# Kernel tuning notes

Measured on AMD Instinct MI355X. Metric: run time of the kernel, lower is better.

The kernel has to match this reference:

```python
import math
import jax, jax.numpy as jnp
import numpy as np

DIM = 1024
QK_DIM = 200
HIDDEN = 2 * DIM  # expansion_factor = 2
N = 8192


def setup_inputs() -> dict:
    key = jax.random.key(0)
    ks = jax.random.split(key, 8)
    s = 0.02
    return {
        "x": jax.random.normal(ks[0], (N, DIM), dtype=jnp.float32),
        "W_hidden": jax.random.normal(ks[1], (DIM, 2 * HIDDEN), dtype=jnp.float32) * s,
        "b_hidden": jnp.zeros((2 * HIDDEN,), dtype=jnp.float32),
        "W_qk": jax.random.normal(ks[2], (DIM, QK_DIM), dtype=jnp.float32) * s,
        "b_qk": jnp.zeros((QK_DIM,), dtype=jnp.float32),
        "gamma": 1.0 + jax.random.normal(ks[3], (2, QK_DIM), dtype=jnp.float32) * s,
        "beta": jnp.zeros((2, QK_DIM), dtype=jnp.float32),
        "W_out": jax.random.normal(ks[4], (HIDDEN, DIM), dtype=jnp.float32) * s,
        "b_out": jnp.zeros((DIM,), dtype=jnp.float32),
    }


def reference(x, W_hidden, b_hidden, W_qk, b_qk, gamma, beta, W_out, b_out):
    # to_hidden: Linear(dim -> 2*hidden) + SiLU, then chunk into v, gate
    hid = jax.nn.silu(x @ W_hidden + b_hidden)        # [N, 2H]
    v, gate = jnp.split(hid, 2, axis=-1)              # [N, H] each
    # to_qk: Linear(dim -> qk_dim) + SiLU
    qk = jax.nn.silu(x @ W_qk + b_qk)                 # [N, qk]
    # OffsetScale (heads=2): per-head affine on the shared qk
    q = qk * gamma[0] + beta[0]                       # [N, qk]
    k = qk * gamma[1] + beta[1]                       # [N, qk]
    # scores scaled by sqrt(dim) (module uses self.dim, not qk_dim)
    sim = (q @ k.T) * (1.0 / math.sqrt(x.shape[-1]))  # [N, N]
    # ReLU-squared attention (no softmax); dropout=0.0 -> identity
    attn = jnp.square(jax.nn.relu(sim))
    out = attn @ v                                    # [N, H]
    out = out * gate
    out = out @ W_out + b_out                         # [N, dim]
    # add_residual=True in this module multiplies by x
    return out * x
```

## Files before the change

kernel.cpp:

```cpp
#include <hip/hip_runtime.h>
#include <stdint.h>


typedef __bf16 bf16x8 __attribute__((ext_vector_type(8)));
typedef float f32x4 __attribute__((ext_vector_type(4)));

__device__ __forceinline__ uint16_t f2bf(float f) {
  uint32_t u = __builtin_bit_cast(uint32_t, f);
  u += 0x7fffu + ((u >> 16) & 1u);
  return (uint16_t)(u >> 16);
}
__device__ __forceinline__ float silu_f(float s) {
  return s / (1.f + __expf(-s));
}

__device__ __forceinline__ void gload16(const void* g, void* l) {
  __builtin_amdgcn_global_load_lds(
      (__attribute__((address_space(1))) void*)const_cast<void*>(g),
      (__attribute__((address_space(3))) void*)l, 16, 0, 0);
}


__global__ void cast_to_bf16(const float* __restrict__ in, uint16_t* __restrict__ out, int n4) {
  int i = blockIdx.x * blockDim.x + threadIdx.x;
  if (i < n4) {
    float4 f = ((const float4*)in)[i];
    ushort4 o;
    o.x = f2bf(f.x); o.y = f2bf(f.y); o.z = f2bf(f.z); o.w = f2bf(f.w);
    ((ushort4*)out)[i] = o;
  }
}

__global__ void transpose_cast_pad(const float* __restrict__ in, uint16_t* __restrict__ out,
                                   int R, int C, int Cp) {
  __shared__ float tile[32][33];
  int cb = blockIdx.x * 32;
  int rb = blockIdx.y * 32;
  int tx = threadIdx.x;
  int ty = threadIdx.y;
#pragma unroll
  for (int i = 0; i < 4; ++i) {
    int r = rb + ty + i * 8;
    int c = cb + tx;
    tile[ty + i * 8][tx] = (c < C) ? in[(size_t)r * C + c] : 0.f;
  }
  __syncthreads();
#pragma unroll
  for (int i = 0; i < 4; ++i) {
    int c = cb + ty + i * 8;
    if (c < Cp) out[(size_t)c * R + rb + tx] = f2bf(tile[tx][ty + i * 8]);
  }
}

__global__ void k_sum(uint16_t* __restrict__ P0, const uint16_t* __restrict__ P1,
                      const uint16_t* __restrict__ g, int n8) {
  int i = blockIdx.x * blockDim.x + threadIdx.x;
  if (i < n8) {
    bf16x8 a = ((const bf16x8*)P0)[i];
    bf16x8 b = ((const bf16x8*)P1)[i];
    bf16x8 gg = ((const bf16x8*)g)[i];
    bf16x8 o;
#pragma unroll
    for (int e = 0; e < 8; ++e)
      o[e] = (__bf16)(((float)a[e] + (float)b[e]) * (float)gg[e]);
    ((bf16x8*)P0)[i] = o;
  }
}


struct EpiParams {
  const float* bias;
  const float* bias2;
  const float* g0;
  const float* b0;
  const float* g1;
  const float* b1;
  const uint16_t* gate;
  const float* x;
  uint16_t* o16a;
  uint16_t* o16b;
  uint16_t* oq;
  uint16_t* ok;
  float* o32;
};

#define ET(T_, WS_, RS_, CA_, CB_, NA_, NB_)                                   \
  do {                                                                         \
    const int kp_ = (((T_) + 3) & (NT - 1)) * 32;                              \
    uint16_t* sd_ = SH + (WS_) * 16384 + wave * 512;                           \
    gload16(gA0 + kp_, sd_);                                                   \
    gload16(gA1 + kp_, sd_ + 4096);                                            \
    gload16(gB0 + kp_, sd_ + 8192);                                            \
    gload16(gB1 + kp_, sd_ + 12288);                                           \
    const uint16_t* rb_ = SH + (RS_) * 16384;                                  \
    _Pragma("unroll") for (int j_ = 0; j_ < 4; ++j_)                           \
        NB_[j_] = *(const bf16x8*)(rb_ + rdB + j_ * 512);                      \
    _Pragma("unroll") for (int i_ = 0; i_ < 8; ++i_)                           \
        NA_[i_] = *(const bf16x8*)(rb_ + rdA + i_ * 512);                      \
    __builtin_amdgcn_sched_barrier(0);                                         \
    __builtin_amdgcn_s_setprio(1);                                             \
    _Pragma("unroll") for (int i_ = 0; i_ < 8; ++i_)                           \
      _Pragma("unroll") for (int j_ = 0; j_ < 4; ++j_)                         \
          acc[i_][j_] = __builtin_amdgcn_mfma_f32_16x16x32_bf16(               \
              CA_[i_], CB_[j_], acc[i_][j_], 0, 0, 0);                         \
    __builtin_amdgcn_s_setprio(0);                                             \
    asm volatile("s_waitcnt vmcnt(4)" ::: "memory");                           \
    __builtin_amdgcn_sched_barrier(0);                                         \
    __builtin_amdgcn_s_barrier();                                              \
    __builtin_amdgcn_sched_barrier(0);                                         \
  } while (0)

#define ENGINE256()                                                            \
  do {                                                                         \
    _Pragma("unroll") for (int s_ = 0; s_ < 3; ++s_) {                         \
      uint16_t* d_ = SH + s_ * 16384 + wave * 512;                             \
      gload16(gA0 + s_ * 32, d_);                                              \
      gload16(gA1 + s_ * 32, d_ + 4096);                                       \
      gload16(gB0 + s_ * 32, d_ + 8192);                                       \
      gload16(gB1 + s_ * 32, d_ + 12288);                                      \
    }                                                                          \
    asm volatile("s_waitcnt vmcnt(4)" ::: "memory");                           \
    __builtin_amdgcn_sched_barrier(0);                                         \
    __builtin_amdgcn_s_barrier();                                              \
    __builtin_amdgcn_sched_barrier(0);                                         \
    _Pragma("unroll") for (int j_ = 0; j_ < 4; ++j_)                           \
        fb0[j_] = *(const bf16x8*)(SH + rdB + j_ * 512);                       \
    _Pragma("unroll") for (int i_ = 0; i_ < 8; ++i_)                           \
        fa0[i_] = *(const bf16x8*)(SH + rdA + i_ * 512);                       \
    for (int t0_ = 0; t0_ < NT; t0_ += 4) {                                    \
      ET(t0_ + 0, 3, 1, fa0, fb0, fa1, fb1);                                   \
      ET(t0_ + 1, 0, 2, fa1, fb1, fa0, fb0);                                   \
      ET(t0_ + 2, 1, 3, fa0, fb0, fa1, fb1);                                   \
      ET(t0_ + 3, 2, 0, fa1, fb1, fa0, fb0);                                   \
    }                                                                          \
    asm volatile("s_waitcnt vmcnt(0)" ::: "memory");                           \
    __builtin_amdgcn_sched_barrier(0);                                         \
    __syncthreads();                                                           \
  } while (0)

#define TILE128(T_, B_, BS_)                                                   \
  do {                                                                         \
    const uint16_t* base_ = SH + (B_) * 8192;                                  \
    const int kp_ = (((T_) + 3) & (NT - 1)) * 32;                              \
    uint16_t* sd_ = SH + (BS_) * 8192 + wave * 512;                            \
    gload16(gA0 + kp_, sd_);                                                   \
    gload16(gA1 + kp_, sd_ + 2048);                                            \
    gload16(gB0 + kp_, sd_ + 4096);                                            \
    gload16(gB1 + kp_, sd_ + 6144);                                            \
    bf16x8 a_[4], b_[4];                                                       \
    _Pragma("unroll") for (int j_ = 0; j_ < 4; ++j_)                           \
        b_[j_] = *(const bf16x8*)(base_ + rdB + j_ * 512);                     \
    _Pragma("unroll") for (int i_ = 0; i_ < 4; ++i_)                           \
        a_[i_] = *(const bf16x8*)(base_ + rdA + i_ * 512);                     \
    __builtin_amdgcn_s_setprio(1);                                             \
    _Pragma("unroll") for (int i_ = 0; i_ < 4; ++i_)                           \
      _Pragma("unroll") for (int j_ = 0; j_ < 4; ++j_)                         \
          acc[i_][j_] = __builtin_amdgcn_mfma_f32_16x16x32_bf16(               \
              a_[i_], b_[j_], acc[i_][j_], 0, 0, 0);                           \
    __builtin_amdgcn_s_setprio(0);                                             \
    asm volatile("s_waitcnt vmcnt(8)" ::: "memory");                           \
    __builtin_amdgcn_sched_barrier(0);                                         \
    __builtin_amdgcn_s_barrier();                                              \
    __builtin_amdgcn_sched_barrier(0);                                         \
  } while (0)

#define RING_LOOP128()                                                         \
  do {                                                                         \
    _Pragma("unroll") for (int s_ = 0; s_ < 3; ++s_) {                         \
      uint16_t* d_ = SH + s_ * 8192 + wave * 512;                              \
      gload16(gA0 + s_ * 32, d_);                                              \
      gload16(gA1 + s_ * 32, d_ + 2048);                                       \
      gload16(gB0 + s_ * 32, d_ + 4096);                                       \
      gload16(gB1 + s_ * 32, d_ + 6144);                                       \
    }                                                                          \
    asm volatile("s_waitcnt vmcnt(8)" ::: "memory");                           \
    __builtin_amdgcn_sched_barrier(0);                                         \
    __builtin_amdgcn_s_barrier();                                              \
    __builtin_amdgcn_sched_barrier(0);                                         \
    for (int t0_ = 0; t0_ < NT; t0_ += 4) {                                    \
      TILE128(t0_ + 0, 0, 3);                                                  \
      TILE128(t0_ + 1, 1, 0);                                                  \
      TILE128(t0_ + 2, 2, 1);                                                  \
      TILE128(t0_ + 3, 3, 2);                                                  \
    }                                                                          \
    asm volatile("s_waitcnt vmcnt(0)" ::: "memory");                           \
    __builtin_amdgcn_sched_barrier(0);                                         \
    __syncthreads();                                                           \
  } while (0)

__global__ __launch_bounds__(512, 2) void k_hidqk(
    const uint16_t* __restrict__ A, const uint16_t* __restrict__ Bt, EpiParams p) {
  __shared__ __align__(16) uint16_t SH[65536];

  const int tid = threadIdx.x;
  const int lane = tid & 63;
  const int wave = tid >> 6;
  const int wrM = (wave >> 2) * 128;
  const int wcN = (wave & 3) * 64;
  const int m0 = blockIdx.y * 256;
  const int n0 = blockIdx.x * 256;
  const int lda = 1024, ldb = 1024;
  const int NT = 32;

  f32x4 acc[8][4] = {};

  const int fr = lane & 15;
  const int rg = lane >> 4;
  const int swz = (rg ^ ((fr >> 1) & 3)) * 8;
  const int rdA = (wrM + fr) * 32 + swz;
  const int rdB = 8192 + (wcN + fr) * 32 + swz;

  const int srow = lane >> 2;
  const int sk = ((lane & 3) ^ ((lane >> 3) & 3)) * 8;
  const uint16_t* gA0 = A + (size_t)(m0 + wave * 16 + srow) * lda + sk;
  const uint16_t* gA1 = gA0 + (size_t)128 * lda;
  const uint16_t* gB0 = Bt + (size_t)(n0 + wave * 16 + srow) * ldb + sk;
  const uint16_t* gB1 = gB0 + (size_t)128 * ldb;

  bf16x8 fa0[8], fb0[4], fa1[8], fb1[4];
  ENGINE256();

  if (n0 < 2048) {
    uint16_t* ar = SH + wave * 2304;
#pragma unroll
    for (int j = 0; j < 4; ++j) {
      const float bc = p.bias[n0 + wcN + j * 16 + fr];
#pragma unroll
      for (int i = 0; i < 8; ++i)
#pragma unroll
        for (int r = 0; r < 4; ++r)
          ar[fr * 136 + i * 16 + rg * 4 + r] = f2bf(silu_f(acc[i][j][r] + bc));
      const int mc = (lane & 15) * 8;
#pragma unroll
      for (int it = 0; it < 4; ++it) {
        const int nrow = it * 4 + (lane >> 4);
        bf16x8 v = *(const bf16x8*)(ar + nrow * 136 + mc);
        *(bf16x8*)(p.o16a + (size_t)(n0 + wcN + j * 16 + nrow) * 8192 + m0 + wrM + mc) = v;
      }
    }
  } else if (n0 < 4096) {
    uint16_t* ar = SH + wave * 2048;
    const int lrow = lane >> 3;
    const int nc = (lane & 7) * 8;
    float bc[4];
#pragma unroll
    for (int j = 0; j < 4; ++j) bc[j] = p.bias[n0 + wcN + j * 16 + fr];
#pragma unroll
    for (int i = 0; i < 8; ++i) {
#pragma unroll
      for (int j = 0; j < 4; ++j)
#pragma unroll
        for (int r = 0; r < 4; ++r)
          ar[(rg * 4 + r) * 72 + j * 16 + fr] = f2bf(silu_f(acc[i][j][r] + bc[j]));
#pragma unroll
      for (int rr = 0; rr < 2; ++rr) {
        bf16x8 v = *(const bf16x8*)(ar + (rr * 8 + lrow) * 72 + nc);
        *(bf16x8*)(p.o16b + (size_t)(m0 + wrM + i * 16 + rr * 8 + lrow) * 2048 + (n0 - 2048) + wcN + nc) = v;
      }
    }
  } else {
#pragma unroll
    for (int i = 0; i < 8; ++i) {
#pragma unroll
      for (int j = 0; j < 4; ++j) {
        const int row = m0 + wrM + i * 16 + rg * 4;
        const int qc = wcN + j * 16 + fr;
#pragma unroll
        for (int r = 0; r < 4; ++r) {
          float qv = 0.f, kv = 0.f;
          if (qc < 200) {
            float s = silu_f(acc[i][j][r] + p.bias2[qc]);
            qv = s * p.g0[qc] + p.b0[qc];
            kv = s * p.g1[qc] + p.b1[qc];
          }
          p.oq[(size_t)(row + r) * 256 + qc] = f2bf(qv);
          p.ok[(size_t)(row + r) * 256 + qc] = f2bf(kv);
        }
      }
    }
  }
}

__global__ __launch_bounds__(512, 2) void k_attn(
    const uint16_t* __restrict__ Q,
    const uint16_t* __restrict__ Kt,
    uint16_t* __restrict__ attn) {
  __shared__ __align__(16) uint16_t SH[65536];

  const int tid = threadIdx.x;
  const int lane = tid & 63;
  const int wave = tid >> 6;
  const int wrM = (wave >> 2) * 128;
  const int wcN = (wave & 3) * 64;
  const int m0 = blockIdx.y * 256;
  const int n0 = blockIdx.x * 256;
  const int lda = 256, ldb = 256;
  const int NT = 8;

  f32x4 acc[8][4] = {};

  const int fr = lane & 15;
  const int rg = lane >> 4;
  const int swz = (rg ^ ((fr >> 1) & 3)) * 8;
  const int rdA = (wrM + fr) * 32 + swz;
  const int rdB = 8192 + (wcN + fr) * 32 + swz;

  const int srow = lane >> 2;
  const int sk = ((lane & 3) ^ ((lane >> 3) & 3)) * 8;
  const uint16_t* gA0 = Q + (size_t)(m0 + wave * 16 + srow) * lda + sk;
  const uint16_t* gA1 = gA0 + (size_t)128 * lda;
  const uint16_t* gB0 = Kt + (size_t)(n0 + wave * 16 + srow) * ldb + sk;
  const uint16_t* gB1 = gB0 + (size_t)128 * ldb;

  bf16x8 fa0[8], fb0[4], fa1[8], fb1[4];
  ENGINE256();

  uint16_t* ar = SH + wave * 2048;
  const int row = lane >> 2;
  const int c0 = (lane & 3) * 16;
#pragma unroll
  for (int i = 0; i < 8; ++i) {
#pragma unroll
    for (int j = 0; j < 4; ++j)
#pragma unroll
      for (int r = 0; r < 4; ++r) {
        float s = fmaxf(acc[i][j][r] * 0.03125f, 0.f);
        ar[(rg * 4 + r) * 72 + j * 16 + fr] = f2bf(s * s);
      }
    bf16x8 v0 = *(const bf16x8*)(ar + row * 72 + c0);
    bf16x8 v1 = *(const bf16x8*)(ar + row * 72 + c0 + 8);
    uint16_t* dst = attn + (size_t)(m0 + wrM + i * 16 + row) * 8192 + (n0 + wcN + c0);
    *(bf16x8*)(dst) = v0;
    *(bf16x8*)(dst + 8) = v1;
  }
}

__global__ __launch_bounds__(512, 2) void k_pv(
    const uint16_t* __restrict__ A,
    const uint16_t* __restrict__ Bt,
    uint16_t* __restrict__ P0,
    uint16_t* __restrict__ P1,
    const uint16_t* __restrict__ gate,
    int split) {
  __shared__ __align__(16) uint16_t SH[65536];

  const int id = blockIdx.x;
  int bx, by, kv0, NT;
  uint16_t* dst;
  if (split) {
    bx = id & 7;
    by = id >> 4;
    kv0 = ((id >> 3) & 1) * 4096;
    NT = 128;
    dst = ((id >> 3) & 1) ? P1 : P0;
  } else {
    bx = (id >> 3) & 7;
    by = (id & 7) + 8 * (id >> 6);
    kv0 = 0;
    NT = 256;
    dst = P0;
  }
  const int m0 = by * 256;
  const int n0 = bx * 256;

  const int tid = threadIdx.x;
  const int lane = tid & 63;
  const int wave = tid >> 6;
  const int wrM = (wave >> 2) * 128;
  const int wcN = (wave & 3) * 64;

  const int fr = lane & 15;
  const int rg = lane >> 4;
  const int swz = (rg ^ ((fr >> 1) & 3)) * 8;
  const int rdA = (wrM + fr) * 32 + swz;
  const int rdB = 8192 + (wcN + fr) * 32 + swz;

  const int srow = lane >> 2;
  const int sk = ((lane & 3) ^ ((lane >> 3) & 3)) * 8;
  const uint16_t* gA0 = A + (size_t)(m0 + wave * 16 + srow) * 8192 + kv0 + sk;
  const uint16_t* gA1 = gA0 + (size_t)128 * 8192;
  const uint16_t* gB0 = Bt + (size_t)(n0 + wave * 16 + srow) * 8192 + kv0 + sk;
  const uint16_t* gB1 = gB0 + (size_t)128 * 8192;

  f32x4 acc[8][4] = {};
  bf16x8 fa0[8], fb0[4], fa1[8], fb1[4];
  ENGINE256();

  uint16_t* ar = SH + wave * 2048;
  const int lrow = lane >> 3;
  const int nc = (lane & 7) * 8;
#pragma unroll
  for (int i = 0; i < 8; ++i) {
#pragma unroll
    for (int j = 0; j < 4; ++j)
#pragma unroll
      for (int r = 0; r < 4; ++r)
        ar[(rg * 4 + r) * 72 + j * 16 + fr] = f2bf(acc[i][j][r]);
#pragma unroll
    for (int rr = 0; rr < 2; ++rr) {
      const size_t base = (size_t)(m0 + wrM + i * 16 + rr * 8 + lrow) * 2048 + n0 + wcN + nc;
      bf16x8 v = *(const bf16x8*)(ar + (rr * 8 + lrow) * 72 + nc);
      if (gate) {
        bf16x8 g = *(const bf16x8*)(gate + base);
        bf16x8 o;
#pragma unroll
        for (int e = 0; e < 8; ++e) o[e] = (__bf16)((float)v[e] * (float)g[e]);
        *(bf16x8*)(dst + base) = o;
      } else {
        *(bf16x8*)(dst + base) = v;
      }
    }
  }
}

__global__ __launch_bounds__(256, 2) void k_final(
    const uint16_t* __restrict__ A,
    const uint16_t* __restrict__ Bt, EpiParams p) {
  __shared__ __align__(16) uint16_t SH[32768];

  const int tid = threadIdx.x;
  const int lane = tid & 63;
  const int wave = tid >> 6;
  const int wr = (wave >> 1) * 64;
  const int wc = (wave & 1) * 64;
  const int m0 = blockIdx.y * 128;
  const int n0 = blockIdx.x * 128;
  const int lda = 2048, ldb = 2048;
  const int NT = 64;

  f32x4 acc[4][4] = {};

  const int fr = lane & 15;
  const int rg = lane >> 4;
  const int swz = (rg ^ ((fr >> 1) & 3)) * 8;
  const int rdA = (wr + fr) * 32 + swz;
  const int rdB = 4096 + (wc + fr) * 32 + swz;

  const int srow = lane >> 2;
  const int sk = ((lane & 3) ^ ((lane >> 3) & 3)) * 8;
  const uint16_t* gA0 = A + (size_t)(m0 + wave * 16 + srow) * lda + sk;
  const uint16_t* gA1 = gA0 + (size_t)64 * lda;
  const uint16_t* gB0 = Bt + (size_t)(n0 + wave * 16 + srow) * ldb + sk;
  const uint16_t* gB1 = gB0 + (size_t)64 * ldb;

  RING_LOOP128();

#pragma unroll
  for (int i = 0; i < 4; ++i) {
#pragma unroll
    for (int j = 0; j < 4; ++j) {
      const int row = m0 + wr + i * 16 + rg * 4;
      const int col = n0 + wc + j * 16 + fr;
      const float bc = p.bias[col];
#pragma unroll
      for (int r = 0; r < 4; ++r) {
        size_t idx = (size_t)(row + r) * 1024 + col;
        p.o32[idx] = (acc[i][j][r] + bc) * p.x[idx];
      }
    }
  }
}


extern "C" void kernel_launch(void* const* d_in, const int* in_sizes, int n_in,
                              void* d_out, int out_size, void* d_ws, size_t ws_size,
                              hipStream_t stream) {
  const float* x        = (const float*)d_in[0];
  const float* W_hidden = (const float*)d_in[1];
  const float* b_hidden = (const float*)d_in[2];
  const float* W_qk     = (const float*)d_in[3];
  const float* b_qk     = (const float*)d_in[4];
  const float* gamma    = (const float*)d_in[5];
  const float* beta     = (const float*)d_in[6];
  const float* W_out    = (const float*)d_in[7];
  const float* b_out    = (const float*)d_in[8];
  float* out = (float*)d_out;

  const bool fullM = ws_size >= (236ull << 20);
  const size_t region0 = fullM ? (128ull << 20) : (64ull << 20);

  char* base = (char*)d_ws;
  uint16_t* xb    = (uint16_t*)(base);
  uint16_t* WhT   = (uint16_t*)(base + (16ull << 20));
  uint16_t* WqkT  = (uint16_t*)(base + (24ull << 20));
  uint16_t* attnB = (uint16_t*)(base);
  char* tail = base + region0;
  uint16_t* WoT   = (uint16_t*)(tail);
  uint16_t* q     = (uint16_t*)(tail + (4ull << 20));
  uint16_t* kk    = (uint16_t*)(tail + (8ull << 20));
  uint16_t* vT    = (uint16_t*)(tail + (12ull << 20));
  uint16_t* gate  = (uint16_t*)(tail + (44ull << 20));
  uint16_t* out2g = (uint16_t*)(tail + (76ull << 20));
  (void)in_sizes; (void)n_in; (void)out_size;

  cast_to_bf16<<<(8192 * 1024 / 4) / 256, 256, 0, stream>>>(x, xb, 8192 * 1024 / 4);
  transpose_cast_pad<<<dim3(4096 / 32, 1024 / 32), dim3(32, 8), 0, stream>>>(W_hidden, WhT, 1024, 4096, 4096);
  transpose_cast_pad<<<dim3(256 / 32, 1024 / 32), dim3(32, 8), 0, stream>>>(W_qk, WqkT, 1024, 200, 256);
  transpose_cast_pad<<<dim3(1024 / 32, 2048 / 32), dim3(32, 8), 0, stream>>>(W_out, WoT, 2048, 1024, 1024);

  {
    EpiParams p{};
    p.bias = b_hidden; p.bias2 = b_qk;
    p.g0 = gamma; p.b0 = beta; p.g1 = gamma + 200; p.b1 = beta + 200;
    p.o16a = vT; p.o16b = gate; p.oq = q; p.ok = kk;
    k_hidqk<<<dim3(17, 32), 512, 0, stream>>>(xb, WhT, p);
  }

  if (fullM) {
    k_attn<<<dim3(32, 32), 512, 0, stream>>>(q, kk, attnB);
    k_pv<<<dim3(256), 512, 0, stream>>>(attnB, vT, out2g, nullptr, gate, 0);
    EpiParams p{};
    p.bias = b_out; p.x = x; p.o32 = out;
    k_final<<<dim3(8, 64), 256, 0, stream>>>(out2g, WoT, p);
  } else {
    const size_t PH = 4096ull * 2048;
    for (int s = 0; s < 2; ++s) {
      k_attn<<<dim3(32, 16), 512, 0, stream>>>(q + (size_t)s * 4096 * 256, kk, attnB);
      uint16_t* Pa = out2g + (size_t)s * PH;
      uint16_t* Pb = out2g + (size_t)(1 - s) * PH;
      k_pv<<<dim3(256), 512, 0, stream>>>(attnB, vT, Pa, Pb, nullptr, 1);
      k_sum<<<dim3((int)(PH / 8 / 256)), 256, 0, stream>>>(
          Pa, Pb, gate + (size_t)s * PH, (int)(PH / 8));
      EpiParams p{};
      p.bias = b_out;
      p.x = x + (size_t)s * 4096 * 1024;
      p.o32 = out + (size_t)s * 4096 * 1024;
      k_final<<<dim3(8, 32), 256, 0, stream>>>(Pa, WoT, p);
    }
  }
}
```

Before: 607.2 us.

## Widen k_pv K-tile to 64 with XOR-swizzled double-buffered LDS pipeline

Replaces the ENGINE256 macro in the PV GEMM kernel with an inline loop that stages 64-wide K slices of A and Bt into LDS through global_load_lds, double-buffering over the 64K-element shared array. The iteration count halves, which is meant to halve the per-iteration barrier and wait overhead. Each iteration issues two 32-wide MFMA sub-steps using an 8-way XOR swizzle to avoid bank conflicts, with setprio raised around the MFMAs. The cost is the full 128KB of LDS, which may limit occupancy, and a vmcnt(0) wait at the end of every iteration that could expose load latency.

```diff
diff --git a/kernel.cpp b/kernel.cpp
--- a/kernel.cpp
+++ b/kernel.cpp
@@ -351,13 +351,13 @@
     bx = id & 7;
     by = id >> 4;
     kv0 = ((id >> 3) & 1) * 4096;
-    NT = 128;
+    NT = 64;
     dst = ((id >> 3) & 1) ? P1 : P0;
   } else {
     bx = (id >> 3) & 7;
     by = (id & 7) + 8 * (id >> 6);
     kv0 = 0;
-    NT = 256;
+    NT = 128;
     dst = P0;
   }
   const int m0 = by * 256;
@@ -371,20 +371,78 @@
 
   const int fr = lane & 15;
   const int rg = lane >> 4;
-  const int swz = (rg ^ ((fr >> 1) & 3)) * 8;
-  const int rdA = (wrM + fr) * 32 + swz;
-  const int rdB = 8192 + (wcN + fr) * 32 + swz;
-
-  const int srow = lane >> 2;
-  const int sk = ((lane & 3) ^ ((lane >> 3) & 3)) * 8;
-  const uint16_t* gA0 = A + (size_t)(m0 + wave * 16 + srow) * 8192 + kv0 + sk;
-  const uint16_t* gA1 = gA0 + (size_t)128 * 8192;
-  const uint16_t* gB0 = Bt + (size_t)(n0 + wave * 16 + srow) * 8192 + kv0 + sk;
-  const uint16_t* gB1 = gB0 + (size_t)128 * 8192;
+  const int fr7 = fr & 7;
+  const int octr0 = ((0 * 4 + rg) ^ fr7) * 8;
+  const int octr1 = ((1 * 4 + rg) ^ fr7) * 8;
+  const int rdA0 = (wrM + fr) * 64;
+  const int rdB0 = 16384 + (wcN + fr) * 64;
+
+  const int srow8 = lane >> 3;
+  const int soct = ((lane & 7) ^ srow8) * 8;
+  const uint16_t* gA = A + (size_t)(m0 + wave * 32 + srow8) * 8192 + kv0 + soct;
+  const uint16_t* gB = Bt + (size_t)(n0 + wave * 32 + srow8) * 8192 + kv0 + soct;
 
   f32x4 acc[8][4] = {};
-  bf16x8 fa0[8], fb0[4], fa1[8], fb1[4];
-  ENGINE256();
+
+#pragma unroll
+  for (int g = 0; g < 4; ++g) {
+    gload16(gA + (size_t)(g * 8) * 8192, SH + (wave * 32 + g * 8) * 64);
+    gload16(gB + (size_t)(g * 8) * 8192, SH + 16384 + (wave * 32 + g * 8) * 64);
+  }
+  asm volatile("s_waitcnt vmcnt(0)" ::: "memory");
+  __builtin_amdgcn_sched_barrier(0);
+  __builtin_amdgcn_s_barrier();
+  __builtin_amdgcn_sched_barrier(0);
+
+  for (int t = 0; t < NT; ++t) {
+    const int cur = t & 1;
+    const int kn = ((t + 1) & (NT - 1)) * 64;
+    uint16_t* sd = SH + (cur ^ 1) * 32768;
+#pragma unroll
+    for (int g = 0; g < 4; ++g) {
+      gload16(gA + kn + (size_t)(g * 8) * 8192, sd + (wave * 32 + g * 8) * 64);
+      gload16(gB + kn + (size_t)(g * 8) * 8192, sd + 16384 + (wave * 32 + g * 8) * 64);
+    }
+    const uint16_t* sb = SH + cur * 32768;
+    {
+      bf16x8 aq[8], bq[4];
+#pragma unroll
+      for (int j = 0; j < 4; ++j)
+        bq[j] = *(const bf16x8*)(sb + rdB0 + j * 1024 + octr0);
+#pragma unroll
+      for (int i = 0; i < 8; ++i)
+        aq[i] = *(const bf16x8*)(sb + rdA0 + i * 1024 + octr0);
+      __builtin_amdgcn_s_setprio(1);
+#pragma unroll
+      for (int i = 0; i < 8; ++i)
+#pragma unroll
+        for (int j = 0; j < 4; ++j)
+          acc[i][j] = __builtin_amdgcn_mfma_f32_16x16x32_bf16(
+              aq[i], bq[j], acc[i][j], 0, 0, 0);
+      __builtin_amdgcn_s_setprio(0);
+    }
+    {
+      bf16x8 aq[8], bq[4];
+#pragma unroll
+      for (int j = 0; j < 4; ++j)
+        bq[j] = *(const bf16x8*)(sb + rdB0 + j * 1024 + octr1);
+#pragma unroll
+      for (int i = 0; i < 8; ++i)
+        aq[i] = *(const bf16x8*)(sb + rdA0 + i * 1024 + octr1);
+      __builtin_amdgcn_s_setprio(1);
+#pragma unroll
+      for (int i = 0; i < 8; ++i)
+#pragma unroll
+        for (int j = 0; j < 4; ++j)
+          acc[i][j] = __builtin_amdgcn_mfma_f32_16x16x32_bf16(
+              aq[i], bq[j], acc[i][j], 0, 0, 0);
+      __builtin_amdgcn_s_setprio(0);
+    }
+    asm volatile("s_waitcnt vmcnt(0)" ::: "memory");
+    __builtin_amdgcn_sched_barrier(0);
+    __builtin_amdgcn_s_barrier();
+    __builtin_amdgcn_sched_barrier(0);
+  }
 
   uint16_t* ar = SH + wave * 2048;
   const int lrow = lane >> 3;
```

Measured after the change: 613.7 us. About the same (+1.1%).

## Restructure GEMM main loop into split-phase interleave and fuse prep kernels

Applied to the files above, without the earlier changes.

Replaces the register double-buffered main loop (8 A + 4 B fragments held for the next tile) with a single-buffered loop. Each K step is split into two halves of A fragments, with global-to-LDS loads and barriers interleaved between the halves, which lowers VGPR pressure and spreads memory issue across compute. The loop is no longer unrolled and allows more outstanding loads (vmcnt 8). Separately, the cast kernel and the three weight transpose kernels are merged into one launch to cut launch overhead, at the cost of extra barriers per K step in the GEMM loop.

```diff
diff --git a/kernel.cpp b/kernel.cpp
--- a/kernel.cpp
+++ b/kernel.cpp
@@ -21,23 +21,12 @@
 }
 
 
-__global__ void cast_to_bf16(const float* __restrict__ in, uint16_t* __restrict__ out, int n4) {
-  int i = blockIdx.x * blockDim.x + threadIdx.x;
-  if (i < n4) {
-    float4 f = ((const float4*)in)[i];
-    ushort4 o;
-    o.x = f2bf(f.x); o.y = f2bf(f.y); o.z = f2bf(f.z); o.w = f2bf(f.w);
-    ((ushort4*)out)[i] = o;
-  }
-}
-
-__global__ void transpose_cast_pad(const float* __restrict__ in, uint16_t* __restrict__ out,
-                                   int R, int C, int Cp) {
+__device__ __forceinline__ void transpose_body(
+    const float* __restrict__ in, uint16_t* __restrict__ out,
+    int R, int C, int Cp, int bx, int by, int tx, int ty) {
   __shared__ float tile[32][33];
-  int cb = blockIdx.x * 32;
-  int rb = blockIdx.y * 32;
-  int tx = threadIdx.x;
-  int ty = threadIdx.y;
+  int cb = bx * 32;
+  int rb = by * 32;
 #pragma unroll
   for (int i = 0; i < 4; ++i) {
     int r = rb + ty + i * 8;
@@ -49,6 +38,32 @@
   for (int i = 0; i < 4; ++i) {
     int c = cb + ty + i * 8;
     if (c < Cp) out[(size_t)c * R + rb + tx] = f2bf(tile[tx][ty + i * 8]);
+  }
+}
+
+__global__ __launch_bounds__(256) void k_prep(
+    const float* __restrict__ x, uint16_t* __restrict__ xb,
+    const float* __restrict__ Wh, uint16_t* __restrict__ WhT,
+    const float* __restrict__ Wqk, uint16_t* __restrict__ WqkT,
+    const float* __restrict__ Wo, uint16_t* __restrict__ WoT) {
+  const int id = blockIdx.x;
+  const int tid = threadIdx.x;
+  const int tx = tid & 31, ty = tid >> 5;
+  if (id < 8192) {
+    int i = id * 256 + tid;
+    float4 f = ((const float4*)x)[i];
+    ushort4 o;
+    o.x = f2bf(f.x); o.y = f2bf(f.y); o.z = f2bf(f.z); o.w = f2bf(f.w);
+    ((ushort4*)xb)[i] = o;
+  } else if (id < 12288) {
+    int l = id - 8192;
+    transpose_body(Wh, WhT, 1024, 4096, 4096, l & 127, l >> 7, tx, ty);
+  } else if (id < 12544) {
+    int l = id - 12288;
+    transpose_body(Wqk, WqkT, 1024, 200, 256, l & 7, l >> 3, tx, ty);
+  } else {
+    int l = id - 12544;
+    transpose_body(Wo, WoT, 2048, 1024, 1024, l & 31, l >> 5, tx, ty);
   }
 }
 
@@ -84,27 +99,44 @@
   float* o32;
 };
 
-#define ET(T_, WS_, RS_, CA_, CB_, NA_, NB_)                                   \
+#define ET(T_)                                                                 \
   do {                                                                         \
+    const uint16_t* rb_ = SH + ((T_) & 3) * 16384;                             \
+    uint16_t* sd_ = SH + (((T_) + 3) & 3) * 16384 + wave * 512;                \
     const int kp_ = (((T_) + 3) & (NT - 1)) * 32;                              \
-    uint16_t* sd_ = SH + (WS_) * 16384 + wave * 512;                           \
+    bf16x8 a_[4], b_[4];                                                       \
+    _Pragma("unroll") for (int j_ = 0; j_ < 4; ++j_)                           \
+        b_[j_] = *(const bf16x8*)(rb_ + rdB + j_ * 512);                       \
+    _Pragma("unroll") for (int i_ = 0; i_ < 4; ++i_)                           \
+        a_[i_] = *(const bf16x8*)(rb_ + rdA + i_ * 512);                       \
     gload16(gA0 + kp_, sd_);                                                   \
     gload16(gA1 + kp_, sd_ + 4096);                                            \
+    __builtin_amdgcn_sched_barrier(0);                                         \
+    __builtin_amdgcn_s_barrier();                                              \
+    __builtin_amdgcn_sched_barrier(0);                                         \
+    __builtin_amdgcn_s_setprio(1);                                             \
+    _Pragma("unroll") for (int i_ = 0; i_ < 4; ++i_)                           \
+      _Pragma("unroll") for (int j_ = 0; j_ < 4; ++j_)                         \
+          acc[i_][j_] = __builtin_amdgcn_mfma_f32_16x16x32_bf16(               \
+              a_[i_], b_[j_], acc[i_][j_], 0, 0, 0);                           \
+    __builtin_amdgcn_s_setprio(0);                                             \
+    __builtin_amdgcn_sched_barrier(0);                                         \
+    __builtin_amdgcn_s_barrier();                                              \
+    __builtin_amdgcn_sched_barrier(0);                                         \
+    _Pragma("unroll") for (int i_ = 0; i_ < 4; ++i_)                           \
+        a_[i_] = *(const bf16x8*)(rb_ + rdA + (4 + i_) * 512);                 \
     gload16(gB0 + kp_, sd_ + 8192);                                            \
     gload16(gB1 + kp_, sd_ + 12288);                                           \
-    const uint16_t* rb_ = SH + (RS_) * 16384;                                  \
-    _Pragma("unroll") for (int j_ = 0; j_ < 4; ++j_)                           \
-        NB_[j_] = *(const bf16x8*)(rb_ + rdB + j_ * 512);                      \
-    _Pragma("unroll") for (int i_ = 0; i_ < 8; ++i_)                           \
-        NA_[i_] = *(const bf16x8*)(rb_ + rdA + i_ * 512);                      \
+    __builtin_amdgcn_sched_barrier(0);                                         \
+    __builtin_amdgcn_s_barrier();                                              \
     __builtin_amdgcn_sched_barrier(0);                                         \
     __builtin_amdgcn_s_setprio(1);                                             \
-    _Pragma("unroll") for (int i_ = 0; i_ < 8; ++i_)                           \
+    _Pragma("unroll") for (int i_ = 0; i_ < 4; ++i_)                           \
       _Pragma("unroll") for (int j_ = 0; j_ < 4; ++j_)                         \
-          acc[i_][j_] = __builtin_amdgcn_mfma_f32_16x16x32_bf16(               \
-              CA_[i_], CB_[j_], acc[i_][j_], 0, 0, 0);                         \
+          acc[4 + i_][j_] = __builtin_amdgcn_mfma_f32_16x16x32_bf16(           \
+              a_[i_], b_[j_], acc[4 + i_][j_], 0, 0, 0);                       \
     __builtin_amdgcn_s_setprio(0);                                             \
-    asm volatile("s_waitcnt vmcnt(4)" ::: "memory");                           \
+    asm volatile("s_waitcnt vmcnt(8)" ::: "memory");                           \
     __builtin_amdgcn_sched_barrier(0);                                         \
     __builtin_amdgcn_s_barrier();                                              \
     __builtin_amdgcn_sched_barrier(0);                                         \
@@ -119,20 +151,11 @@
       gload16(gB0 + s_ * 32, d_ + 8192);                                       \
       gload16(gB1 + s_ * 32, d_ + 12288);                                      \
     }                                                                          \
-    asm volatile("s_waitcnt vmcnt(4)" ::: "memory");                           \
-    __builtin_amdgcn_sched_barrier(0);                                         \
-    __builtin_amdgcn_s_barrier();                                              \
-    __builtin_amdgcn_sched_barrier(0);                                         \
-    _Pragma("unroll") for (int j_ = 0; j_ < 4; ++j_)                           \
-        fb0[j_] = *(const bf16x8*)(SH + rdB + j_ * 512);                       \
-    _Pragma("unroll") for (int i_ = 0; i_ < 8; ++i_)                           \
-        fa0[i_] = *(const bf16x8*)(SH + rdA + i_ * 512);                       \
-    for (int t0_ = 0; t0_ < NT; t0_ += 4) {                                    \
-      ET(t0_ + 0, 3, 1, fa0, fb0, fa1, fb1);                                   \
-      ET(t0_ + 1, 0, 2, fa1, fb1, fa0, fb0);                                   \
-      ET(t0_ + 2, 1, 3, fa0, fb0, fa1, fb1);                                   \
-      ET(t0_ + 3, 2, 0, fa1, fb1, fa0, fb0);                                   \
-    }                                                                          \
+    asm volatile("s_waitcnt vmcnt(8)" ::: "memory");                           \
+    __builtin_amdgcn_sched_barrier(0);                                         \
+    __builtin_amdgcn_s_barrier();                                              \
+    __builtin_amdgcn_sched_barrier(0);                                         \
+    _Pragma("unroll 1") for (int t_ = 0; t_ < NT; ++t_) ET(t_);                \
     asm volatile("s_waitcnt vmcnt(0)" ::: "memory");                           \
     __builtin_amdgcn_sched_barrier(0);                                         \
     __syncthreads();                                                           \
@@ -217,7 +240,6 @@
   const uint16_t* gB0 = Bt + (size_t)(n0 + wave * 16 + srow) * ldb + sk;
   const uint16_t* gB1 = gB0 + (size_t)128 * ldb;
 
-  bf16x8 fa0[8], fb0[4], fa1[8], fb1[4];
   ENGINE256();
 
   if (n0 < 2048) {
@@ -312,7 +334,6 @@
   const uint16_t* gB0 = Kt + (size_t)(n0 + wave * 16 + srow) * ldb + sk;
   const uint16_t* gB1 = gB0 + (size_t)128 * ldb;
 
-  bf16x8 fa0[8], fb0[4], fa1[8], fb1[4];
   ENGINE256();
 
   uint16_t* ar = SH + wave * 2048;
@@ -383,7 +404,6 @@
   const uint16_t* gB1 = gB0 + (size_t)128 * 8192;
 
   f32x4 acc[8][4] = {};
-  bf16x8 fa0[8], fb0[4], fa1[8], fb1[4];
   ENGINE256();
 
   uint16_t* ar = SH + wave * 2048;
@@ -493,10 +513,7 @@
   uint16_t* out2g = (uint16_t*)(tail + (76ull << 20));
   (void)in_sizes; (void)n_in; (void)out_size;
 
-  cast_to_bf16<<<(8192 * 1024 / 4) / 256, 256, 0, stream>>>(x, xb, 8192 * 1024 / 4);
-  transpose_cast_pad<<<dim3(4096 / 32, 1024 / 32), dim3(32, 8), 0, stream>>>(W_hidden, WhT, 1024, 4096, 4096);
-  transpose_cast_pad<<<dim3(256 / 32, 1024 / 32), dim3(32, 8), 0, stream>>>(W_qk, WqkT, 1024, 200, 256);
-  transpose_cast_pad<<<dim3(1024 / 32, 2048 / 32), dim3(32, 8), 0, stream>>>(W_out, WoT, 2048, 1024, 1024);
+  k_prep<<<dim3(14592), 256, 0, stream>>>(x, xb, W_hidden, WhT, W_qk, WqkT, W_out, WoT);
 
   {
     EpiParams p{};
```

New measurement: 605.5 us. Within noise of the previous version (-0.3%).
